# Kernel tuning notes

Hardware: AMD Instinct MI355X
Metric: run time of the kernel (lower is better)

## Reference

```python
import jax, jax.numpy as jnp
import numpy as np

B, N, D, H, HID, EN = 2, 4096, 128, 4, 32, 16
ALPHA = 0.2           # LeakyReLU slope
NEG = -9e15           # masked_fill value from the original code


def setup_inputs() -> dict:
    key = jax.random.key(0)
    ks = jax.random.split(key, 6)
    fea = jax.random.normal(ks[0], (B, N, D), dtype=jnp.float32)
    # binary dense adjacency (regulon x gene), square here so narrow() is identity
    adj = jax.random.randint(ks[1], (B, N, N), 0, 2).astype(jnp.float32)
    # per-head GAT params (xavier-ish scale)
    W_heads = jax.random.normal(ks[2], (H, D, HID), dtype=jnp.float32) * 0.1
    a_heads = jax.random.normal(ks[3], (H, 2 * HID, 1), dtype=jnp.float32) * 0.1
    W_last = jax.random.normal(ks[4], (H * HID, EN), dtype=jnp.float32) * 0.1
    a_last = jax.random.normal(ks[5], (2 * EN, 1), dtype=jnp.float32) * 0.1
    return {"fea_mats": fea, "adj_mats": adj, "W_heads": W_heads,
            "a_heads": a_heads, "W_last": W_last, "a_last": a_last}


def _gat_layer(x, adj, W, a, concat):
    # x: [N, d_in], adj: [nr, N], W: [d_in, out], a: [2*out, 1]
    out_dim = W.shape[1]
    wh = x @ W                                   # [N, out]
    nr = adj.shape[0]
    wh1 = wh[:nr] @ a[:out_dim]                  # [nr, 1]
    wh2 = wh @ a[out_dim:]                       # [N, 1]
    e = jax.nn.leaky_relu(wh1 + wh2.T, ALPHA)    # [nr, N]
    # _prepare_attentions: mask by adj, weight by adj, fill zeros with -9e15
    att = jnp.where(adj != 0, e * adj, 0.0)
    att = jnp.where(att == 0, NEG, att)
    att = jax.nn.softmax(att, axis=1)
    # the original detaches attention via a numpy roundtrip
    att = jax.lax.stop_gradient(att)
    res = att @ wh                               # [nr, out]
    return jax.nn.elu(res) if concat else res


def reference(fea_mats, adj_mats, W_heads, a_heads, W_last, a_last):
    def per_sample(x, adj):
        # multi-head attention layers (concat=True), vmapped over heads
        heads = jax.vmap(lambda W, a: _gat_layer(x, adj, W, a, True))(W_heads, a_heads)  # [H, N, HID]
        xcat = jnp.transpose(heads, (1, 0, 2)).reshape(x.shape[0], H * HID)  # torch.cat(dim=1)
        nr = adj.shape[0]
        out = _gat_layer(xcat, adj[:, :nr], W_last, a_last, False)  # adj.narrow(1,0,nr)
        return jax.nn.elu(out)  # [N, EN]
    return jax.vmap(per_sample)(fea_mats, adj_mats)  # [B, N, EN]
```

## Files before the change

kernel.cpp:

```cpp
#include <hip/hip_runtime.h>
#include <hip/hip_bf16.h>
#include <stdint.h>

#define B_ 2
#define N_ 4096
#define D_ 128
#define H_ 4
#define HID_ 32
#define EN_ 16
#define ALPHA_ 0.2f
#define S1_ 4
#define S2_ 4
#define LOG2E_ 1.4426950408889634f

typedef __attribute__((ext_vector_type(8))) _Float16 f16x8;
typedef __attribute__((ext_vector_type(4))) float f32x4;
typedef __attribute__((ext_vector_type(8))) unsigned short u16x8;

__device__ __forceinline__ unsigned short f2h(float v) {
    _Float16 h = (_Float16)v;
    return *(unsigned short*)&h;
}

__global__ __launch_bounds__(256) void maskc_kernel(
    const float* __restrict__ adj, unsigned long long* __restrict__ mask)
{
    const int b = blockIdx.y;
    const int i = blockIdx.x * 4 + (threadIdx.x >> 6);
    const int lane = threadIdx.x & 63;
    const float* ar = adj + ((size_t)b * N_ + i) * N_;
    unsigned long long* mrow = mask + ((size_t)b * N_ + i) * 64;
#pragma unroll 4
    for (int c = 0; c < 16; ++c) {
        float4 v = *(const float4*)(ar + c * 256 + lane * 4);
        unsigned long long b0 = __ballot(v.x != 0.f);
        unsigned long long b1 = __ballot(v.y != 0.f);
        unsigned long long b2 = __ballot(v.z != 0.f);
        unsigned long long b3 = __ballot(v.w != 0.f);
        if (lane == 0) {
            ulonglong2 w01 = {b0, b1}, w23 = {b2, b3};
            *(ulonglong2*)(mrow + c * 4) = w01;
            *(ulonglong2*)(mrow + c * 4 + 2) = w23;
        }
    }
}

__global__ __launch_bounds__(256) void proj1_kernel(
    const float* __restrict__ fea, const float* __restrict__ Wh,
    const float* __restrict__ a_heads,
    float* __restrict__ wh1, float* __restrict__ wh2,
    float* __restrict__ cmax1, unsigned short* __restrict__ whTt)
{
    __shared__ float Ws[D_ * HID_];
    __shared__ float xs[8][D_];
    __shared__ float as_[2 * HID_];
    __shared__ unsigned short ts[HID_][8];
    __shared__ float rmax[8];
    const int b = blockIdx.z, h = blockIdx.y, i0 = blockIdx.x * 8, tid = threadIdx.x;
    const float* Wp = Wh + h * D_ * HID_;
    for (int idx = tid * 4; idx < D_ * HID_; idx += 1024)
        *(float4*)&Ws[idx] = *(const float4*)(Wp + idx);
    const float* xp = fea + ((size_t)b * N_ + i0) * D_;
    *(float4*)&xs[(tid * 4) >> 7][(tid * 4) & 127] = *(const float4*)(xp + tid * 4);
    if (tid < 2 * HID_) as_[tid] = a_heads[h * 2 * HID_ + tid];
    __syncthreads();
    const int r = tid >> 5, d = tid & 31;
    float acc = 0.f;
#pragma unroll 8
    for (int k = 0; k < D_; ++k) acc += xs[r][k] * Ws[k * HID_ + d];
    ts[d][r] = f2h(acc);
    float d1 = acc * as_[d], d2 = acc * as_[HID_ + d];
#pragma unroll
    for (int off = 16; off; off >>= 1) {
        d1 += __shfl_xor(d1, off);
        d2 += __shfl_xor(d2, off);
    }
    d1 *= LOG2E_; d2 *= LOG2E_;
    if (d == 0) {
        const size_t o = (size_t)(b * H_ + h) * N_ + i0 + r;
        wh1[o] = d1; wh2[o] = d2; rmax[r] = d2;
    }
    __syncthreads();
    if (tid < HID_) {
        unsigned short* dst = whTt + (size_t)(b * H_ + h) * 131072
                            + (i0 >> 6) * 2048 + tid * 64 + (i0 & 63);
        *(u16x8*)dst = *(u16x8*)&ts[tid][0];
    }
    if (tid == 0) {
        float mx = rmax[0];
#pragma unroll
        for (int k = 1; k < 8; ++k) mx = fmaxf(mx, rmax[k]);
        cmax1[(size_t)(b * H_ + h) * 512 + blockIdx.x] = mx;
    }
}

__global__ __launch_bounds__(256) void attn1_kernel(
    const unsigned long long* __restrict__ mask, const unsigned short* __restrict__ whT,
    const float* __restrict__ wh1, const float* __restrict__ wh2,
    const float* __restrict__ cmax1,
    float* __restrict__ x2p, float* __restrict__ l1p)
{
    __shared__ unsigned long long mask_s[16][18];
    const int b = blockIdx.z, split = blockIdx.y, i0 = blockIdx.x * 16;
    const int tid = threadIdx.x, lane = tid & 63, h = tid >> 6;
    const int m = lane & 15, quad = lane >> 4;
    mask_s[tid >> 4][tid & 15] =
        mask[((size_t)b * N_ + i0 + (tid >> 4)) * 64 + split * 16 + (tid & 15)];
    const float* cm = cmax1 + (size_t)(b * H_ + h) * 512;
    float4 c0 = *(const float4*)(cm + lane * 8);
    float4 c1 = *(const float4*)(cm + lane * 8 + 4);
    float Mh = fmaxf(fmaxf(fmaxf(c0.x, c0.y), fmaxf(c0.z, c0.w)),
                     fmaxf(fmaxf(c1.x, c1.y), fmaxf(c1.z, c1.w)));
#pragma unroll
    for (int off = 32; off; off >>= 1) Mh = fmaxf(Mh, __shfl_xor(Mh, off));
    const float w1r = wh1[(size_t)(b * H_ + h) * N_ + i0 + m];
    const float sbound = w1r + Mh;
    const float mr = fmaxf(sbound, ALPHA_ * sbound);
    const float* w2h = wh2 + (size_t)(b * H_ + h) * N_;
    const unsigned short* whTp = whT + (size_t)(b * H_ + h) * 131072;
    f32x4 acc0 = {0.f, 0.f, 0.f, 0.f}, acc1 = {0.f, 0.f, 0.f, 0.f};
    f32x4 acc2 = {0.f, 0.f, 0.f, 0.f};
    f16x8 ones;
#pragma unroll
    for (int q = 0; q < 8; ++q) ones[q] = (_Float16)1.0f;
    const int jt0 = split * (N_ / S1_);
    __syncthreads();

    for (int c = 0; c < 4; ++c) {
        unsigned long long W0 = mask_s[m][c * 4 + 0], W1 = mask_s[m][c * 4 + 1];
        unsigned long long W2 = mask_s[m][c * 4 + 2], W3 = mask_s[m][c * 4 + 3];
#pragma unroll
        for (int q4 = 0; q4 < 4; ++q4) {
            const int t = c * 4 + q4;
            const int jt = jt0 + t * 64;
            const int jb = split * 16 + t;
#pragma unroll
            for (int ks = 0; ks < 2; ++ks) {
                const int ko = ks * 32 + quad * 8;
                const int sh = 16 * q4 + 8 * ks + 2 * quad;
                unsigned int g0 = (unsigned int)(W0 >> sh) & 3u;
                unsigned int g1 = (unsigned int)(W1 >> sh) & 3u;
                unsigned int g2 = (unsigned int)(W2 >> sh) & 3u;
                unsigned int g3 = (unsigned int)(W3 >> sh) & 3u;
                float wv8[8];
                *(float4*)&wv8[0] = *(const float4*)(w2h + jt + ko);
                *(float4*)&wv8[4] = *(const float4*)(w2h + jt + ko + 4);
                f16x8 af;
#pragma unroll
                for (int q = 0; q < 4; ++q) {
                    float p2[2];
#pragma unroll
                    for (int cc = 0; cc < 2; ++cc) {
                        const int jj = q * 2 + cc;
                        unsigned int gw = (jj & 3) == 0 ? g0 : (jj & 3) == 1 ? g1
                                        : (jj & 3) == 2 ? g2 : g3;
                        unsigned int bit = gw & (1u << (jj >> 2));
                        float s = w1r + wv8[jj];
                        float e = fmaxf(s, ALPHA_ * s);
                        float tt = (bit == 0u || s == 0.f) ? -1e38f : (e - mr);
                        p2[cc] = __builtin_amdgcn_exp2f(tt);
                    }
                    auto pr = __builtin_amdgcn_cvt_pkrtz(p2[0], p2[1]);
                    af[q * 2] = (_Float16)pr[0]; af[q * 2 + 1] = (_Float16)pr[1];
                }
                const unsigned short* bp = whTp + (size_t)jb * 2048 + m * 64 + ko;
                f16x8 b0 = *(const f16x8*)bp;
                f16x8 b1 = *(const f16x8*)(bp + 1024);
                acc0 = __builtin_amdgcn_mfma_f32_16x16x32_f16(af, b0, acc0, 0, 0, 0);
                acc1 = __builtin_amdgcn_mfma_f32_16x16x32_f16(af, b1, acc1, 0, 0, 0);
                acc2 = __builtin_amdgcn_mfma_f32_16x16x32_f16(af, ones, acc2, 0, 0, 0);
            }
        }
    }
    float* xp = x2p + (((size_t)split * B_ + b) * N_ + i0) * D_ + h * HID_;
#pragma unroll
    for (int reg = 0; reg < 4; ++reg) {
        const int row = quad * 4 + reg;
        xp[(size_t)row * D_ + m] = acc0[reg];
        xp[(size_t)row * D_ + 16 + m] = acc1[reg];
    }
    if (m == 0) {
#pragma unroll
        for (int reg = 0; reg < 4; ++reg)
            l1p[(((size_t)split * B_ + b) * N_ + i0 + quad * 4 + reg) * H_ + h] = acc2[reg];
    }
}

__global__ __launch_bounds__(256) void proj2_kernel(
    const float* __restrict__ x2p, const float* __restrict__ l1p,
    const float* __restrict__ Wl, const float* __restrict__ a_last,
    float* __restrict__ wh1b, float* __restrict__ wh2b,
    float* __restrict__ cmax2, unsigned short* __restrict__ whT2t)
{
    __shared__ float Ws[D_ * EN_];
    __shared__ float xs[16][D_];
    __shared__ float as_[2 * EN_];
    __shared__ unsigned short ts[EN_][16];
    __shared__ float rmax[16];
    const int b = blockIdx.y, i0 = blockIdx.x * 16, tid = threadIdx.x;
    for (int idx = tid * 4; idx < D_ * EN_; idx += 1024)
        *(float4*)&Ws[idx] = *(const float4*)(Wl + idx);
    if (tid < 2 * EN_) as_[tid] = a_last[tid];
    for (int idx = tid * 4; idx < 16 * D_; idx += 1024) {
        const int r = idx >> 7, hd = idx & 127, h = hd >> 5;
        float4 v = {0.f, 0.f, 0.f, 0.f};
        float l = 0.f;
#pragma unroll
        for (int s = 0; s < S1_; ++s) {
            const size_t gi = ((size_t)s * B_ + b) * N_ + i0 + r;
            float4 p = *(const float4*)(x2p + gi * D_ + hd);
            v.x += p.x; v.y += p.y; v.z += p.z; v.w += p.w;
            l += l1p[gi * H_ + h];
        }
        float linv = 1.f / fmaxf(l, 1e-30f);
        float o0 = v.x * linv, o1 = v.y * linv, o2 = v.z * linv, o3 = v.w * linv;
        xs[r][hd]     = o0 > 0.f ? o0 : expm1f(o0);
        xs[r][hd + 1] = o1 > 0.f ? o1 : expm1f(o1);
        xs[r][hd + 2] = o2 > 0.f ? o2 : expm1f(o2);
        xs[r][hd + 3] = o3 > 0.f ? o3 : expm1f(o3);
    }
    __syncthreads();
    const int r = tid >> 4, e = tid & 15;
    float acc = 0.f;
#pragma unroll 8
    for (int k = 0; k < D_; ++k) acc += xs[r][k] * Ws[k * EN_ + e];
    ts[e][r] = f2h(acc);
    float d1 = acc * as_[e], d2 = acc * as_[EN_ + e];
#pragma unroll
    for (int off = 8; off; off >>= 1) {
        d1 += __shfl_xor(d1, off);
        d2 += __shfl_xor(d2, off);
    }
    d1 *= LOG2E_; d2 *= LOG2E_;
    if (e == 0) {
        wh1b[(size_t)b * N_ + i0 + r] = d1;
        wh2b[(size_t)b * N_ + i0 + r] = d2;
        rmax[r] = d2;
    }
    __syncthreads();
    if (tid < EN_) {
        unsigned short* dst = whT2t + (size_t)b * 65536
                            + (i0 >> 6) * 1024 + tid * 64 + (i0 & 63);
        *(u16x8*)dst = *(u16x8*)&ts[tid][0];
        *(u16x8*)(dst + 8) = *(u16x8*)&ts[tid][8];
    }
    if (tid == 0) {
        float mx = rmax[0];
#pragma unroll
        for (int k = 1; k < 16; ++k) mx = fmaxf(mx, rmax[k]);
        cmax2[(size_t)b * 256 + blockIdx.x] = mx;
    }
}

__global__ __launch_bounds__(256) void attn2_kernel(
    const unsigned long long* __restrict__ mask, const unsigned short* __restrict__ whT2,
    const float* __restrict__ wh1b, const float* __restrict__ wh2b,
    const float* __restrict__ cmax2,
    float* __restrict__ outp, float* __restrict__ outlp)
{
    __shared__ unsigned long long mask_s[16][18];
    __shared__ float accred[4][16][17];
    __shared__ float lred[4][16];
    const int b = blockIdx.z, split = blockIdx.y, i0 = blockIdx.x * 16;
    const int tid = threadIdx.x, lane = tid & 63, wv = tid >> 6;
    const int m = lane & 15, quad = lane >> 4;
    mask_s[tid >> 4][tid & 15] =
        mask[((size_t)b * N_ + i0 + (tid >> 4)) * 64 + split * 16 + (tid & 15)];
    const float* cm = cmax2 + (size_t)b * 256;
    float4 c0 = *(const float4*)(cm + lane * 4);
    float Mh = fmaxf(fmaxf(c0.x, c0.y), fmaxf(c0.z, c0.w));
#pragma unroll
    for (int off = 32; off; off >>= 1) Mh = fmaxf(Mh, __shfl_xor(Mh, off));
    const float w1r = wh1b[(size_t)b * N_ + i0 + m];
    const float sbound = w1r + Mh;
    const float mr = fmaxf(sbound, ALPHA_ * sbound);
    const float* w2g = wh2b + (size_t)b * N_;
    const unsigned short* wTg = whT2 + (size_t)b * 65536;
    f32x4 acc = {0.f, 0.f, 0.f, 0.f}, acc2 = {0.f, 0.f, 0.f, 0.f};
    f16x8 ones;
#pragma unroll
    for (int q = 0; q < 8; ++q) ones[q] = (_Float16)1.0f;
    const int jt0 = split * (N_ / S2_);
    __syncthreads();
    unsigned long long W0 = mask_s[m][wv * 4 + 0], W1 = mask_s[m][wv * 4 + 1];
    unsigned long long W2 = mask_s[m][wv * 4 + 2], W3 = mask_s[m][wv * 4 + 3];
#pragma unroll
    for (int q4 = 0; q4 < 4; ++q4) {
        const int t = wv * 4 + q4;
        const int jt = jt0 + t * 64;
        const int jb = split * 16 + t;
#pragma unroll
        for (int ks = 0; ks < 2; ++ks) {
            const int ko = ks * 32 + quad * 8;
            const int sh = 16 * q4 + 8 * ks + 2 * quad;
            unsigned int g0 = (unsigned int)(W0 >> sh) & 3u;
            unsigned int g1 = (unsigned int)(W1 >> sh) & 3u;
            unsigned int g2 = (unsigned int)(W2 >> sh) & 3u;
            unsigned int g3 = (unsigned int)(W3 >> sh) & 3u;
            float wv8[8];
            *(float4*)&wv8[0] = *(const float4*)(w2g + jt + ko);
            *(float4*)&wv8[4] = *(const float4*)(w2g + jt + ko + 4);
            f16x8 af;
#pragma unroll
            for (int q = 0; q < 4; ++q) {
                float p2[2];
#pragma unroll
                for (int cc = 0; cc < 2; ++cc) {
                    const int jj = q * 2 + cc;
                    unsigned int gw = (jj & 3) == 0 ? g0 : (jj & 3) == 1 ? g1
                                    : (jj & 3) == 2 ? g2 : g3;
                    unsigned int bit = gw & (1u << (jj >> 2));
                    float s = w1r + wv8[jj];
                    float e = fmaxf(s, ALPHA_ * s);
                    float tt = (bit == 0u || s == 0.f) ? -1e38f : (e - mr);
                    p2[cc] = __builtin_amdgcn_exp2f(tt);
                }
                auto pr = __builtin_amdgcn_cvt_pkrtz(p2[0], p2[1]);
                af[q * 2] = (_Float16)pr[0]; af[q * 2 + 1] = (_Float16)pr[1];
            }
            f16x8 b0 = *(const f16x8*)(wTg + (size_t)jb * 1024 + m * 64 + ko);
            acc = __builtin_amdgcn_mfma_f32_16x16x32_f16(af, b0, acc, 0, 0, 0);
            acc2 = __builtin_amdgcn_mfma_f32_16x16x32_f16(af, ones, acc2, 0, 0, 0);
        }
    }
#pragma unroll
    for (int reg = 0; reg < 4; ++reg)
        accred[wv][quad * 4 + reg][m] = acc[reg];
    if (m == 0) {
#pragma unroll
        for (int reg = 0; reg < 4; ++reg) lred[wv][quad * 4 + reg] = acc2[reg];
    }
    __syncthreads();
    const int row = tid >> 4, col = tid & 15;
    float s = accred[0][row][col] + accred[1][row][col]
            + accred[2][row][col] + accred[3][row][col];
    outp[(((size_t)split * B_ + b) * N_ + i0 + row) * EN_ + col] = s;
    if (tid < 16) {
        float l = lred[0][tid] + lred[1][tid] + lred[2][tid] + lred[3][tid];
        outlp[((size_t)split * B_ + b) * N_ + i0 + tid] = l;
    }
}

__global__ __launch_bounds__(256) void finalize2_kernel(
    const float* __restrict__ outp, const float* __restrict__ outlp,
    float* __restrict__ out)
{
    const int id = blockIdx.x * 256 + threadIdx.x;
    const int gi = id >> 4;
    float num = 0.f, l = 0.f;
#pragma unroll
    for (int s = 0; s < S2_; ++s) {
        num += outp[(size_t)s * B_ * N_ * EN_ + id];
        l   += outlp[(size_t)s * B_ * N_ + gi];
    }
    float v = num / fmaxf(l, 1e-30f);
    out[id] = v > 0.f ? v : expm1f(v);
}

extern "C" void kernel_launch(void* const* d_in, const int* in_sizes, int n_in,
                              void* d_out, int out_size, void* d_ws, size_t ws_size,
                              hipStream_t stream)
{
    const float* fea = (const float*)d_in[0];
    const float* adj = (const float*)d_in[1];
    const float* Wh  = (const float*)d_in[2];
    const float* ah  = (const float*)d_in[3];
    const float* Wl  = (const float*)d_in[4];
    const float* al  = (const float*)d_in[5];

    float* p = (float*)d_ws;
    float* wh1   = p;  p += (size_t)B_ * H_ * N_;
    float* wh2   = p;  p += (size_t)B_ * H_ * N_;
    float* wh1b  = p;  p += (size_t)B_ * N_;
    float* wh2b  = p;  p += (size_t)B_ * N_;
    float* cmax1 = p;  p += (size_t)B_ * H_ * 512;
    float* cmax2 = p;  p += (size_t)B_ * 256;
    float* l1p   = p;  p += (size_t)S1_ * B_ * N_ * H_;
    float* x2p   = p;  p += (size_t)S1_ * B_ * N_ * D_;
    float* outp  = p;  p += (size_t)S2_ * B_ * N_ * EN_;
    float* outlp = p;  p += (size_t)S2_ * B_ * N_;
    unsigned long long* mask = (unsigned long long*)p;
    unsigned short* whTt  = (unsigned short*)(mask + (size_t)B_ * N_ * 64);
    unsigned short* whT2t = whTt + (size_t)B_ * H_ * 131072;

    maskc_kernel<<<dim3(N_ / 4, B_), 256, 0, stream>>>(adj, mask);
    proj1_kernel<<<dim3(N_ / 8, H_, B_), 256, 0, stream>>>(fea, Wh, ah,
                                                           wh1, wh2, cmax1, whTt);
    attn1_kernel<<<dim3(N_ / 16, S1_, B_), 256, 0, stream>>>(mask, whTt, wh1, wh2, cmax1,
                                                             x2p, l1p);
    proj2_kernel<<<dim3(N_ / 16, B_), 256, 0, stream>>>(x2p, l1p, Wl, al,
                                                        wh1b, wh2b, cmax2, whT2t);
    attn2_kernel<<<dim3(N_ / 16, S2_, B_), 256, 0, stream>>>(mask, whT2t, wh1b, wh2b, cmax2,
                                                             outp, outlp);
    finalize2_kernel<<<(B_ * N_ * EN_) / 256, 256, 0, stream>>>(outp, outlp, (float*)d_out);
}
```

Baseline: 327.1 us.

## Retile proj1 to 64 rows, process 32 rows per attn1 block, hoist loads

proj1 now handles 64 rows per block with register-tiled FMA over a transposed W in shared memory, and precomputes W·a so the attention logits come from a direct dot product. attn1 processes 32 query rows per block, so each loaded whT fragment and wh2 vector feeds two MFMA row tiles, halving B-operand global traffic per row. attn1 and attn2 also hoist the B-fragment and wh2 loads ahead of the inner ks loop. The trade-off is higher register pressure in attn1 (six accumulators) and fewer blocks in the grid.

```diff
diff --git a/kernel.cpp b/kernel.cpp
--- a/kernel.cpp
+++ b/kernel.cpp
@@ -51,124 +51,190 @@
     float* __restrict__ wh1, float* __restrict__ wh2,
     float* __restrict__ cmax1, unsigned short* __restrict__ whTt)
 {
-    __shared__ float Ws[D_ * HID_];
-    __shared__ float xs[8][D_];
+    __shared__ float xs[64][132];
+    __shared__ float WT[32][132];
+    __shared__ float Wa[2][128];
     __shared__ float as_[2 * HID_];
-    __shared__ unsigned short ts[HID_][8];
-    __shared__ float rmax[8];
-    const int b = blockIdx.z, h = blockIdx.y, i0 = blockIdx.x * 8, tid = threadIdx.x;
-    const float* Wp = Wh + h * D_ * HID_;
-    for (int idx = tid * 4; idx < D_ * HID_; idx += 1024)
-        *(float4*)&Ws[idx] = *(const float4*)(Wp + idx);
+    __shared__ unsigned short ts[32 * 64];
+    __shared__ float rmax[64];
+    const int b = blockIdx.z, h = blockIdx.y, i0 = blockIdx.x * 64, tid = threadIdx.x;
+    const float* Wp = Wh + (size_t)h * D_ * HID_;
+    for (int l = tid; l < 1024; l += 256) {
+        float4 w4 = *(const float4*)(Wp + l * 4);
+        int k = l >> 3, d = (l & 7) * 4;
+        WT[d][k] = w4.x; WT[d + 1][k] = w4.y; WT[d + 2][k] = w4.z; WT[d + 3][k] = w4.w;
+    }
+    if (tid < 2 * HID_) as_[tid] = a_heads[h * 2 * HID_ + tid];
     const float* xp = fea + ((size_t)b * N_ + i0) * D_;
-    *(float4*)&xs[(tid * 4) >> 7][(tid * 4) & 127] = *(const float4*)(xp + tid * 4);
-    if (tid < 2 * HID_) as_[tid] = a_heads[h * 2 * HID_ + tid];
-    __syncthreads();
-    const int r = tid >> 5, d = tid & 31;
-    float acc = 0.f;
+    for (int l = tid; l < 2048; l += 256) {
+        int r = l >> 5, k4 = (l & 31) * 4;
+        *(float4*)&xs[r][k4] = *(const float4*)(xp + r * D_ + k4);
+    }
+    __syncthreads();
+    {
+        const int k = tid & 127, j = tid >> 7;
+        const float* wr = Wp + k * HID_;
+        const float* aw = &as_[j * HID_];
+        float s = 0.f;
+#pragma unroll
+        for (int d = 0; d < HID_; d += 4) {
+            float4 w4 = *(const float4*)(wr + d);
+            s += w4.x * aw[d] + w4.y * aw[d + 1] + w4.z * aw[d + 2] + w4.w * aw[d + 3];
+        }
+        Wa[j][k] = s;
+    }
+    const int rg = (tid >> 4) * 4, c = tid & 15;
+    float a0[4] = {0.f, 0.f, 0.f, 0.f}, a1[4] = {0.f, 0.f, 0.f, 0.f};
 #pragma unroll 8
-    for (int k = 0; k < D_; ++k) acc += xs[r][k] * Ws[k * HID_ + d];
-    ts[d][r] = f2h(acc);
-    float d1 = acc * as_[d], d2 = acc * as_[HID_ + d];
-#pragma unroll
-    for (int off = 16; off; off >>= 1) {
-        d1 += __shfl_xor(d1, off);
-        d2 += __shfl_xor(d2, off);
-    }
-    d1 *= LOG2E_; d2 *= LOG2E_;
-    if (d == 0) {
-        const size_t o = (size_t)(b * H_ + h) * N_ + i0 + r;
-        wh1[o] = d1; wh2[o] = d2; rmax[r] = d2;
-    }
-    __syncthreads();
-    if (tid < HID_) {
-        unsigned short* dst = whTt + (size_t)(b * H_ + h) * 131072
-                            + (i0 >> 6) * 2048 + tid * 64 + (i0 & 63);
-        *(u16x8*)dst = *(u16x8*)&ts[tid][0];
-    }
-    if (tid == 0) {
-        float mx = rmax[0];
-#pragma unroll
-        for (int k = 1; k < 8; ++k) mx = fmaxf(mx, rmax[k]);
-        cmax1[(size_t)(b * H_ + h) * 512 + blockIdx.x] = mx;
-    }
-}
-
-__global__ __launch_bounds__(256) void attn1_kernel(
+    for (int k = 0; k < D_; k += 4) {
+        float4 w0 = *(float4*)&WT[c][k];
+        float4 w1 = *(float4*)&WT[c + 16][k];
+#pragma unroll
+        for (int i = 0; i < 4; ++i) {
+            float4 x4 = *(float4*)&xs[rg + i][k];
+            a0[i] += x4.x * w0.x + x4.y * w0.y + x4.z * w0.z + x4.w * w0.w;
+            a1[i] += x4.x * w1.x + x4.y * w1.y + x4.z * w1.z + x4.w * w1.w;
+        }
+    }
+#pragma unroll
+    for (int i = 0; i < 4; ++i) {
+        ts[c * 64 + rg + i] = f2h(a0[i]);
+        ts[(c + 16) * 64 + rg + i] = f2h(a1[i]);
+    }
+    __syncthreads();
+    {
+        const int row = tid >> 2, q = tid & 3;
+        float d1 = 0.f, d2 = 0.f;
+#pragma unroll
+        for (int k = q * 32; k < q * 32 + 32; k += 4) {
+            float4 x4 = *(float4*)&xs[row][k];
+            float4 u = *(float4*)&Wa[0][k];
+            float4 v = *(float4*)&Wa[1][k];
+            d1 += x4.x * u.x + x4.y * u.y + x4.z * u.z + x4.w * u.w;
+            d2 += x4.x * v.x + x4.y * v.y + x4.z * v.z + x4.w * v.w;
+        }
+        d1 += __shfl_xor(d1, 1); d1 += __shfl_xor(d1, 2);
+        d2 += __shfl_xor(d2, 1); d2 += __shfl_xor(d2, 2);
+        if (q == 0) {
+            const size_t o = (size_t)(b * H_ + h) * N_ + i0 + row;
+            wh1[o] = d1 * LOG2E_;
+            wh2[o] = d2 * LOG2E_;
+            rmax[row] = d2 * LOG2E_;
+        }
+    }
+    __syncthreads();
+    {
+        unsigned short* dst = whTt + ((size_t)(b * H_ + h) * 64 + blockIdx.x) * 2048;
+        *(u16x8*)(dst + tid * 8) = *(u16x8*)&ts[tid * 8];
+    }
+    if (tid < 64) {
+        float mx = rmax[tid];
+#pragma unroll
+        for (int off = 32; off; off >>= 1) mx = fmaxf(mx, __shfl_xor(mx, off));
+        if (tid == 0) cmax1[(size_t)(b * H_ + h) * 64 + blockIdx.x] = mx;
+    }
+}
+
+__global__ __launch_bounds__(256, 4) void attn1_kernel(
     const unsigned long long* __restrict__ mask, const unsigned short* __restrict__ whT,
     const float* __restrict__ wh1, const float* __restrict__ wh2,
     const float* __restrict__ cmax1,
     float* __restrict__ x2p, float* __restrict__ l1p)
 {
-    __shared__ unsigned long long mask_s[16][18];
-    const int b = blockIdx.z, split = blockIdx.y, i0 = blockIdx.x * 16;
+    __shared__ unsigned long long mask_s[32][17];
+    const int b = blockIdx.z, split = blockIdx.y, i0 = blockIdx.x * 32;
     const int tid = threadIdx.x, lane = tid & 63, h = tid >> 6;
     const int m = lane & 15, quad = lane >> 4;
-    mask_s[tid >> 4][tid & 15] =
-        mask[((size_t)b * N_ + i0 + (tid >> 4)) * 64 + split * 16 + (tid & 15)];
-    const float* cm = cmax1 + (size_t)(b * H_ + h) * 512;
-    float4 c0 = *(const float4*)(cm + lane * 8);
-    float4 c1 = *(const float4*)(cm + lane * 8 + 4);
-    float Mh = fmaxf(fmaxf(fmaxf(c0.x, c0.y), fmaxf(c0.z, c0.w)),
-                     fmaxf(fmaxf(c1.x, c1.y), fmaxf(c1.z, c1.w)));
+    {
+        const int r = tid >> 3, w = (tid & 7) * 2;
+        ulonglong2 mw = *(const ulonglong2*)(mask + ((size_t)b * N_ + i0 + r) * 64
+                                             + split * 16 + w);
+        mask_s[r][w] = mw.x; mask_s[r][w + 1] = mw.y;
+    }
+    const float* cm = cmax1 + (size_t)(b * H_ + h) * 64;
+    float Mh = cm[lane];
 #pragma unroll
     for (int off = 32; off; off >>= 1) Mh = fmaxf(Mh, __shfl_xor(Mh, off));
-    const float w1r = wh1[(size_t)(b * H_ + h) * N_ + i0 + m];
-    const float sbound = w1r + Mh;
-    const float mr = fmaxf(sbound, ALPHA_ * sbound);
-    const float* w2h = wh2 + (size_t)(b * H_ + h) * N_;
-    const unsigned short* whTp = whT + (size_t)(b * H_ + h) * 131072;
-    f32x4 acc0 = {0.f, 0.f, 0.f, 0.f}, acc1 = {0.f, 0.f, 0.f, 0.f};
-    f32x4 acc2 = {0.f, 0.f, 0.f, 0.f};
+    const size_t bhN = (size_t)(b * H_ + h) * N_;
+    const float w1r0 = wh1[bhN + i0 + m];
+    const float w1r1 = wh1[bhN + i0 + 16 + m];
+    const float sb0 = w1r0 + Mh, sb1 = w1r1 + Mh;
+    const float mr0 = fmaxf(sb0, ALPHA_ * sb0);
+    const float mr1 = fmaxf(sb1, ALPHA_ * sb1);
+    const float* wvb = wh2 + bhN + split * 1024 + quad * 8;
+    const unsigned short* bpb = whT + (size_t)(b * H_ + h) * 131072
+                              + (size_t)split * 16 * 2048 + m * 64 + quad * 8;
+    f32x4 a00 = {0.f,0.f,0.f,0.f}, a01 = {0.f,0.f,0.f,0.f}, a02 = {0.f,0.f,0.f,0.f};
+    f32x4 a10 = {0.f,0.f,0.f,0.f}, a11 = {0.f,0.f,0.f,0.f}, a12 = {0.f,0.f,0.f,0.f};
     f16x8 ones;
 #pragma unroll
     for (int q = 0; q < 8; ++q) ones[q] = (_Float16)1.0f;
-    const int jt0 = split * (N_ / S1_);
     __syncthreads();
 
     for (int c = 0; c < 4; ++c) {
-        unsigned long long W0 = mask_s[m][c * 4 + 0], W1 = mask_s[m][c * 4 + 1];
-        unsigned long long W2 = mask_s[m][c * 4 + 2], W3 = mask_s[m][c * 4 + 3];
+        const unsigned long long P0 = mask_s[m][c*4+0], P1 = mask_s[m][c*4+1];
+        const unsigned long long P2 = mask_s[m][c*4+2], P3 = mask_s[m][c*4+3];
+        const unsigned long long Q0 = mask_s[m+16][c*4+0], Q1 = mask_s[m+16][c*4+1];
+        const unsigned long long Q2 = mask_s[m+16][c*4+2], Q3 = mask_s[m+16][c*4+3];
 #pragma unroll
         for (int q4 = 0; q4 < 4; ++q4) {
             const int t = c * 4 + q4;
-            const int jt = jt0 + t * 64;
-            const int jb = split * 16 + t;
+            const unsigned short* bp = bpb + (size_t)t * 2048;
+            f16x8 b00 = *(const f16x8*)bp;
+            f16x8 b10 = *(const f16x8*)(bp + 32);
+            f16x8 b01 = *(const f16x8*)(bp + 1024);
+            f16x8 b11 = *(const f16x8*)(bp + 1056);
+            const float* nw = wvb + t * 64;
+            float4 u0 = *(const float4*)nw;
+            float4 u1 = *(const float4*)(nw + 4);
+            float4 v0 = *(const float4*)(nw + 32);
+            float4 v1 = *(const float4*)(nw + 36);
 #pragma unroll
             for (int ks = 0; ks < 2; ++ks) {
-                const int ko = ks * 32 + quad * 8;
                 const int sh = 16 * q4 + 8 * ks + 2 * quad;
-                unsigned int g0 = (unsigned int)(W0 >> sh) & 3u;
-                unsigned int g1 = (unsigned int)(W1 >> sh) & 3u;
-                unsigned int g2 = (unsigned int)(W2 >> sh) & 3u;
-                unsigned int g3 = (unsigned int)(W3 >> sh) & 3u;
                 float wv8[8];
-                *(float4*)&wv8[0] = *(const float4*)(w2h + jt + ko);
-                *(float4*)&wv8[4] = *(const float4*)(w2h + jt + ko + 4);
-                f16x8 af;
-#pragma unroll
-                for (int q = 0; q < 4; ++q) {
-                    float p2[2];
+                if (ks == 0) { *(float4*)&wv8[0] = u0; *(float4*)&wv8[4] = u1; }
+                else         { *(float4*)&wv8[0] = v0; *(float4*)&wv8[4] = v1; }
+                const unsigned int gp0 = (unsigned int)(P0 >> sh) & 3u;
+                const unsigned int gp1 = (unsigned int)(P1 >> sh) & 3u;
+                const unsigned int gp2 = (unsigned int)(P2 >> sh) & 3u;
+                const unsigned int gp3 = (unsigned int)(P3 >> sh) & 3u;
+                const unsigned int gq0 = (unsigned int)(Q0 >> sh) & 3u;
+                const unsigned int gq1 = (unsigned int)(Q1 >> sh) & 3u;
+                const unsigned int gq2 = (unsigned int)(Q2 >> sh) & 3u;
+                const unsigned int gq3 = (unsigned int)(Q3 >> sh) & 3u;
+                f16x8 af0, af1;
+#pragma unroll
+                for (int qq = 0; qq < 4; ++qq) {
+                    float r0p[2], r1p[2];
 #pragma unroll
                     for (int cc = 0; cc < 2; ++cc) {
-                        const int jj = q * 2 + cc;
-                        unsigned int gw = (jj & 3) == 0 ? g0 : (jj & 3) == 1 ? g1
-                                        : (jj & 3) == 2 ? g2 : g3;
-                        unsigned int bit = gw & (1u << (jj >> 2));
-                        float s = w1r + wv8[jj];
-                        float e = fmaxf(s, ALPHA_ * s);
-                        float tt = (bit == 0u || s == 0.f) ? -1e38f : (e - mr);
-                        p2[cc] = __builtin_amdgcn_exp2f(tt);
+                        const int jj = qq * 2 + cc;
+                        const unsigned int bsel = 1u << (jj >> 2);
+                        const unsigned int gp = (jj&3)==0?gp0:(jj&3)==1?gp1:(jj&3)==2?gp2:gp3;
+                        const unsigned int gq = (jj&3)==0?gq0:(jj&3)==1?gq1:(jj&3)==2?gq2:gq3;
+                        float s0 = w1r0 + wv8[jj];
+                        float e0 = fmaxf(s0, ALPHA_ * s0);
+                        float t0 = ((gp & bsel) == 0u || s0 == 0.f) ? -1e38f : (e0 - mr0);
+                        r0p[cc] = __builtin_amdgcn_exp2f(t0);
+                        float s1 = w1r1 + wv8[jj];
+                        float e1 = fmaxf(s1, ALPHA_ * s1);
+                        float t1 = ((gq & bsel) == 0u || s1 == 0.f) ? -1e38f : (e1 - mr1);
+                        r1p[cc] = __builtin_amdgcn_exp2f(t1);
                     }
-                    auto pr = __builtin_amdgcn_cvt_pkrtz(p2[0], p2[1]);
-                    af[q * 2] = (_Float16)pr[0]; af[q * 2 + 1] = (_Float16)pr[1];
+                    auto pr0 = __builtin_amdgcn_cvt_pkrtz(r0p[0], r0p[1]);
+                    af0[qq*2] = (_Float16)pr0[0]; af0[qq*2+1] = (_Float16)pr0[1];
+                    auto pr1 = __builtin_amdgcn_cvt_pkrtz(r1p[0], r1p[1]);
+                    af1[qq*2] = (_Float16)pr1[0]; af1[qq*2+1] = (_Float16)pr1[1];
                 }
-                const unsigned short* bp = whTp + (size_t)jb * 2048 + m * 64 + ko;
-                f16x8 b0 = *(const f16x8*)bp;
-                f16x8 b1 = *(const f16x8*)(bp + 1024);
-                acc0 = __builtin_amdgcn_mfma_f32_16x16x32_f16(af, b0, acc0, 0, 0, 0);
-                acc1 = __builtin_amdgcn_mfma_f32_16x16x32_f16(af, b1, acc1, 0, 0, 0);
-                acc2 = __builtin_amdgcn_mfma_f32_16x16x32_f16(af, ones, acc2, 0, 0, 0);
+                f16x8 bb0 = ks ? b10 : b00;
+                f16x8 bb1 = ks ? b11 : b01;
+                a00 = __builtin_amdgcn_mfma_f32_16x16x32_f16(af0, bb0, a00, 0, 0, 0);
+                a01 = __builtin_amdgcn_mfma_f32_16x16x32_f16(af0, bb1, a01, 0, 0, 0);
+                a02 = __builtin_amdgcn_mfma_f32_16x16x32_f16(af0, ones, a02, 0, 0, 0);
+                a10 = __builtin_amdgcn_mfma_f32_16x16x32_f16(af1, bb0, a10, 0, 0, 0);
+                a11 = __builtin_amdgcn_mfma_f32_16x16x32_f16(af1, bb1, a11, 0, 0, 0);
+                a12 = __builtin_amdgcn_mfma_f32_16x16x32_f16(af1, ones, a12, 0, 0, 0);
             }
         }
     }
@@ -176,13 +242,18 @@
 #pragma unroll
     for (int reg = 0; reg < 4; ++reg) {
         const int row = quad * 4 + reg;
-        xp[(size_t)row * D_ + m] = acc0[reg];
-        xp[(size_t)row * D_ + 16 + m] = acc1[reg];
+        xp[(size_t)row * D_ + m] = a00[reg];
+        xp[(size_t)row * D_ + 16 + m] = a01[reg];
+        xp[(size_t)(row + 16) * D_ + m] = a10[reg];
+        xp[(size_t)(row + 16) * D_ + 16 + m] = a11[reg];
     }
     if (m == 0) {
-#pragma unroll
-        for (int reg = 0; reg < 4; ++reg)
-            l1p[(((size_t)split * B_ + b) * N_ + i0 + quad * 4 + reg) * H_ + h] = acc2[reg];
+        float* lp = l1p + (((size_t)split * B_ + b) * N_ + i0) * H_ + h;
+#pragma unroll
+        for (int reg = 0; reg < 4; ++reg) {
+            lp[(size_t)(quad * 4 + reg) * H_] = a02[reg];
+            lp[(size_t)(quad * 4 + reg + 16) * H_] = a12[reg];
+        }
     }
 }
 
@@ -284,22 +355,29 @@
     __syncthreads();
     unsigned long long W0 = mask_s[m][wv * 4 + 0], W1 = mask_s[m][wv * 4 + 1];
     unsigned long long W2 = mask_s[m][wv * 4 + 2], W3 = mask_s[m][wv * 4 + 3];
+
+    const unsigned short* wTb = wTg + (size_t)(split * 16 + wv * 4) * 1024 + m * 64 + quad * 8;
+    const float* wvb = w2g + jt0 + wv * 256 + quad * 8;
 #pragma unroll
     for (int q4 = 0; q4 < 4; ++q4) {
-        const int t = wv * 4 + q4;
-        const int jt = jt0 + t * 64;
-        const int jb = split * 16 + t;
+        const unsigned short* bp = wTb + (size_t)q4 * 1024;
+        f16x8 cb0 = *(const f16x8*)(bp);
+        f16x8 cb1 = *(const f16x8*)(bp + 32);
+        const float* nw = wvb + q4 * 64;
+        float4 cu0 = *(const float4*)(nw);
+        float4 cu1 = *(const float4*)(nw + 4);
+        float4 cv0 = *(const float4*)(nw + 32);
+        float4 cv1 = *(const float4*)(nw + 36);
 #pragma unroll
         for (int ks = 0; ks < 2; ++ks) {
-            const int ko = ks * 32 + quad * 8;
             const int sh = 16 * q4 + 8 * ks + 2 * quad;
             unsigned int g0 = (unsigned int)(W0 >> sh) & 3u;
             unsigned int g1 = (unsigned int)(W1 >> sh) & 3u;
             unsigned int g2 = (unsigned int)(W2 >> sh) & 3u;
             unsigned int g3 = (unsigned int)(W3 >> sh) & 3u;
             float wv8[8];
-            *(float4*)&wv8[0] = *(const float4*)(w2g + jt + ko);
-            *(float4*)&wv8[4] = *(const float4*)(w2g + jt + ko + 4);
+            if (ks == 0) { *(float4*)&wv8[0] = cu0; *(float4*)&wv8[4] = cu1; }
+            else         { *(float4*)&wv8[0] = cv0; *(float4*)&wv8[4] = cv1; }
             f16x8 af;
 #pragma unroll
             for (int q = 0; q < 4; ++q) {
@@ -318,8 +396,7 @@
                 auto pr = __builtin_amdgcn_cvt_pkrtz(p2[0], p2[1]);
                 af[q * 2] = (_Float16)pr[0]; af[q * 2 + 1] = (_Float16)pr[1];
             }
-            f16x8 b0 = *(const f16x8*)(wTg + (size_t)jb * 1024 + m * 64 + ko);
-            acc = __builtin_amdgcn_mfma_f32_16x16x32_f16(af, b0, acc, 0, 0, 0);
+            acc = __builtin_amdgcn_mfma_f32_16x16x32_f16(af, ks ? cb1 : cb0, acc, 0, 0, 0);
             acc2 = __builtin_amdgcn_mfma_f32_16x16x32_f16(af, ones, acc2, 0, 0, 0);
         }
     }
@@ -373,7 +450,7 @@
     float* wh2   = p;  p += (size_t)B_ * H_ * N_;
     float* wh1b  = p;  p += (size_t)B_ * N_;
     float* wh2b  = p;  p += (size_t)B_ * N_;
-    float* cmax1 = p;  p += (size_t)B_ * H_ * 512;
+    float* cmax1 = p;  p += (size_t)B_ * H_ * 64;
     float* cmax2 = p;  p += (size_t)B_ * 256;
     float* l1p   = p;  p += (size_t)S1_ * B_ * N_ * H_;
     float* x2p   = p;  p += (size_t)S1_ * B_ * N_ * D_;
@@ -384,9 +461,9 @@
     unsigned short* whT2t = whTt + (size_t)B_ * H_ * 131072;
 
     maskc_kernel<<<dim3(N_ / 4, B_), 256, 0, stream>>>(adj, mask);
-    proj1_kernel<<<dim3(N_ / 8, H_, B_), 256, 0, stream>>>(fea, Wh, ah,
-                                                           wh1, wh2, cmax1, whTt);
-    attn1_kernel<<<dim3(N_ / 16, S1_, B_), 256, 0, stream>>>(mask, whTt, wh1, wh2, cmax1,
+    proj1_kernel<<<dim3(N_ / 64, H_, B_), 256, 0, stream>>>(fea, Wh, ah,
+                                                            wh1, wh2, cmax1, whTt);
+    attn1_kernel<<<dim3(N_ / 32, S1_, B_), 256, 0, stream>>>(mask, whTt, wh1, wh2, cmax1,
                                                              x2p, l1p);
     proj2_kernel<<<dim3(N_ / 16, B_), 256, 0, stream>>>(x2p, l1p, Wl, al,
                                                         wh1b, wh2b, cmax2, whT2t);
```

New measurement: 287.6 us. 1.14x faster.
